# Kernel optimization log

Measured on AMD Instinct MI355X. Metric: run time of the kernel, lower is better.

## Reference

```python
import jax, jax.numpy as jnp
import numpy as np

N = 100000      # entity nodes
E = 1000000     # edges per relation
D_IN = 256
HID = 128
EPS = 1e-16     # PyG softmax denominator eps
NEG_SLOPE = 0.2 # GATConv default leaky_relu slope


def _gat_conv(x, ei, Ws, Wd, a_s, a_d, b):
    """Single-head GATConv (heads=1, concat=False) with self-loops."""
    n = x.shape[0]
    loop = jnp.arange(n, dtype=ei.dtype)
    src = jnp.concatenate([ei[0], loop])  # [E+N]
    dst = jnp.concatenate([ei[1], loop])
    h_src = x @ Ws                         # [N, HID]
    h_dst = x @ Wd                         # [N, HID]
    a_src = h_src @ a_s                    # [N]
    a_dst = h_dst @ a_d                    # [N]
    e = jax.nn.leaky_relu(a_src[src] + a_dst[dst], NEG_SLOPE)  # [E+N]
    # numerically-stable softmax over incoming edges of each dst node
    m = jax.ops.segment_max(e, dst, num_segments=n)
    ex = jnp.exp(e - m[dst])
    denom = jax.ops.segment_sum(ex, dst, num_segments=n)
    alpha = ex / (denom[dst] + EPS)        # [E+N]
    out = jax.ops.segment_sum(alpha[:, None] * h_src[src], dst, num_segments=n)
    return out + b


def setup_inputs() -> dict:
    key = jax.random.key(0)
    ks = jax.random.split(key, 9)
    s_in = 1.0 / np.sqrt(D_IN)
    s_h = 1.0 / np.sqrt(HID)
    return {
        "x": jax.random.normal(ks[0], (N, D_IN), dtype=jnp.float32),
        "edge_index_r0": jax.random.randint(ks[1], (2, E), 0, N, dtype=jnp.int64)
                         if jax.config.jax_enable_x64 else jax.random.randint(ks[1], (2, E), 0, N).astype(jnp.int32),
        "edge_index_r1": jax.random.randint(ks[2], (2, E), 0, N, dtype=jnp.int64)
                         if jax.config.jax_enable_x64 else jax.random.randint(ks[2], (2, E), 0, N).astype(jnp.int32),
        "W_src": jax.random.normal(ks[3], (2, D_IN, HID), dtype=jnp.float32) * s_in,
        "W_dst": jax.random.normal(ks[4], (2, D_IN, HID), dtype=jnp.float32) * s_in,
        "att_src": jax.random.normal(ks[5], (2, HID), dtype=jnp.float32) * s_h,
        "att_dst": jax.random.normal(ks[6], (2, HID), dtype=jnp.float32) * s_h,
        "bias": jnp.zeros((2, HID), dtype=jnp.float32),
    }


def reference(x, edge_index_r0, edge_index_r1, W_src, W_dst, att_src, att_dst, bias):
    # HeteroConv aggr='sum' over the two entity->entity relations
    out = _gat_conv(x, edge_index_r0, W_src[0], W_dst[0], att_src[0], att_dst[0], bias[0])
    out = out + _gat_conv(x, edge_index_r1, W_src[1], W_dst[1], att_src[1], att_dst[1], bias[1])
    # ELU; dropout p=0.0 is identity
    return jax.nn.elu(out)
```

## Files before the change

kernel.cpp:

```cpp
#include <hip/hip_runtime.h>

typedef __attribute__((ext_vector_type(8))) __bf16 bf16x8;
typedef __attribute__((ext_vector_type(4))) float floatx4;
typedef __attribute__((ext_vector_type(2))) float floatx2;

__device__ __forceinline__ float bf2f(unsigned short u) {
    return __uint_as_float(((unsigned)u) << 16);
}
__device__ __forceinline__ unsigned short f2bf(float f) {
    unsigned u = __float_as_uint(f);
    unsigned r = u + 0x7FFFu + ((u >> 16) & 1u);
    return (unsigned short)(r >> 16);
}

__device__ __forceinline__ void canon8(const void* src, unsigned short* dst,
                                       long long idx, int f) {
    if (f) {
        *(uint4*)&dst[idx] = *(const uint4*)((const unsigned short*)src + idx);
    } else {
        const float* sf = (const float*)src;
        unsigned short v[8];
        for (int j = 0; j < 8; ++j) v[j] = f2bf(sf[idx + j]);
        *(uint4*)&dst[idx] = *(const uint4*)v;
    }
}

__global__ __launch_bounds__(256) void detect2_k(
    const unsigned short* __restrict__ xs,
    const void* __restrict__ Ws, const void* __restrict__ Wd,
    const void* __restrict__ as, const void* __restrict__ ad,
    const void* __restrict__ b,
    int* __restrict__ flag, float* __restrict__ vecs,
    unsigned short* __restrict__ bsb) {
    __shared__ int sred[256];
    __shared__ int sflag;
    int tid = threadIdx.x;
    int cnt = 0;
    for (int j = 0; j < 16; ++j) {
        unsigned short u = xs[(tid * 16 + j) * 2];
        int e = (u >> 7) & 0xFF;
        cnt += (e >= 96 && e <= 159) ? 1 : 0;
    }
    sred[tid] = cnt;
    __syncthreads();
    for (int s = 128; s > 0; s >>= 1) {
        if (tid < s) sred[tid] += sred[tid + s];
        __syncthreads();
    }
    if (tid == 0) { sflag = (sred[0] > 2048) ? 1 : 0; *flag = sflag; }
    __syncthreads();
    int f = sflag;
    int k = tid;
    for (int r = 0; r < 2; ++r) {
        float s = 0.f, t = 0.f;
        if (f) {
            const unsigned short* wsrow = (const unsigned short*)Ws + (size_t)r * 32768 + (size_t)k * 128;
            const unsigned short* wdrow = (const unsigned short*)Wd + (size_t)r * 32768 + (size_t)k * 128;
            const unsigned short* asr = (const unsigned short*)as + r * 128;
            const unsigned short* adr = (const unsigned short*)ad + r * 128;
            for (int h = 0; h < 128; ++h) {
                s += bf2f(wsrow[h]) * bf2f(asr[h]);
                t += bf2f(wdrow[h]) * bf2f(adr[h]);
            }
        } else {
            const float* wsrow = (const float*)Ws + (size_t)r * 32768 + (size_t)k * 128;
            const float* wdrow = (const float*)Wd + (size_t)r * 32768 + (size_t)k * 128;
            const float* asr = (const float*)as + r * 128;
            const float* adr = (const float*)ad + r * 128;
            for (int h = 0; h < 128; ++h) {
                s += wsrow[h] * asr[h];
                t += wdrow[h] * adr[h];
            }
        }
        vecs[(r * 2 + 0) * 256 + k] = s;
        vecs[(r * 2 + 1) * 256 + k] = t;
    }
    if (tid < 32) canon8(b, bsb, (long long)tid * 8, f);
}

__global__ __launch_bounds__(256) void mix1_k(
    const int* __restrict__ ei0, const int* __restrict__ ei1,
    int* __restrict__ cntP, int* __restrict__ rank0, int* __restrict__ rank1,
    int E_, int histB, int period,
    const void* __restrict__ xraw, unsigned short* __restrict__ xb,
    const float* __restrict__ vecs, float* __restrict__ aout, int n, int canB,
    unsigned long long* __restrict__ pair0, unsigned long long* __restrict__ pair1,
    int ps2, int zB,
    const void* __restrict__ Ws, unsigned short* __restrict__ Bt,
    const int* __restrict__ flag) {
    __shared__ float sv[1024];
    int b = blockIdx.x, tid = threadIdx.x;
    int bq = b / period;
    if (b - bq * period == 0) {
        if (bq >= histB) return;
        int rel = bq & 1;
        int t = ((bq >> 1) << 8) + tid;
        if (t >= E_ + n) return;
        const int* ei = rel ? ei1 : ei0;
        int* rank = rel ? rank1 : rank0;
        int d = (t < E_) ? ei[E_ + t] : (t - E_);
        rank[t] = atomicAdd(&cntP[((rel ? n : 0) + d) << 4], 1);
        return;
    }
    int oid = b - bq - 1;
    if (oid < canB) {
        for (int j = 0; j < 4; ++j) sv[j * 256 + tid] = vecs[j * 256 + tid];
        __syncthreads();
        int lane = tid & 63, wave = tid >> 6;
        int row = oid * 4 + wave;
        if (row >= n) return;
        float xf[4];
        if (*flag) {
            uint2 u = *(const uint2*)((const unsigned short*)xraw + (size_t)row * 256 + lane * 4);
            xf[0] = bf2f((unsigned short)(u.x & 0xFFFF));
            xf[1] = bf2f((unsigned short)(u.x >> 16));
            xf[2] = bf2f((unsigned short)(u.y & 0xFFFF));
            xf[3] = bf2f((unsigned short)(u.y >> 16));
        } else {
            float4 f = *(const float4*)((const float*)xraw + (size_t)row * 256 + lane * 4);
            xf[0] = f.x; xf[1] = f.y; xf[2] = f.z; xf[3] = f.w;
            unsigned short v[4] = {f2bf(f.x), f2bf(f.y), f2bf(f.z), f2bf(f.w)};
            *(uint2*)&xb[(size_t)row * 256 + lane * 4] = *(const uint2*)v;
        }
        float s[4] = {0.f, 0.f, 0.f, 0.f};
        for (int j = 0; j < 4; ++j)
            for (int q = 0; q < 4; ++q)
                s[j] += xf[q] * sv[j * 256 + lane * 4 + q];
        for (int j = 0; j < 4; ++j)
            for (int off = 32; off > 0; off >>= 1)
                s[j] += __shfl_down(s[j], off);
        if (lane == 0)
            for (int j = 0; j < 4; ++j) aout[(size_t)j * n + row] = s[j];
        return;
    }
    oid -= canB;
    if (oid < 2 * zB) {
        unsigned long long* dst = (oid < zB) ? pair0 : pair1;
        int z = (oid < zB) ? oid : oid - zB;
        int idx = z * 256 + tid;
        if (idx < ps2) ((uint4*)dst)[idx] = make_uint4(0u, 0u, 0u, 0u);
        return;
    }
    oid -= 2 * zB;
    if (oid < 256) {
        int i = oid * 256 + tid;
        int f = *flag;
        int r = i >> 15, rem = i & 32767;
        int k = rem >> 7, nn = rem & 127;
        unsigned short w = f ? ((const unsigned short*)Ws)[i]
                             : f2bf(((const float*)Ws)[i]);
        Bt[(size_t)r * 32768 + nn * 256 + k] = w;
    }
}

__global__ __launch_bounds__(256) void scan_red_k(const int* __restrict__ cntP,
                                                  int* __restrict__ part,
                                                  int n, int nb) {
    __shared__ int s[256];
    int rel = blockIdx.y;
    int i = blockIdx.x * 256 + threadIdx.x;
    int v = (i < n) ? ((cntP[((rel ? n : 0) + i) << 4] + 7) & ~7) : 0;
    s[threadIdx.x] = v;
    __syncthreads();
    for (int o = 128; o > 0; o >>= 1) {
        if (threadIdx.x < o) s[threadIdx.x] += s[threadIdx.x + o];
        __syncthreads();
    }
    if (threadIdx.x == 0) part[rel * nb + blockIdx.x] = s[0];
}

__global__ __launch_bounds__(1024) void scan_mid_k(int* __restrict__ part, int nb) {
    __shared__ int s[1024];
    int rel = blockIdx.x;
    int t = threadIdx.x;
    s[t] = (t < nb) ? part[rel * nb + t] : 0;
    __syncthreads();
    for (int o = 1; o < 1024; o <<= 1) {
        int v = (t >= o) ? s[t - o] : 0;
        __syncthreads();
        s[t] += v;
        __syncthreads();
    }
    if (t < nb) part[rel * nb + t] = (t == 0) ? 0 : s[t - 1];
}

__global__ __launch_bounds__(256) void scan_off_k(const int* __restrict__ cntP,
                                                  const int* __restrict__ part,
                                                  int* __restrict__ off0,
                                                  int* __restrict__ off1,
                                                  int n, int nb) {
    __shared__ int s[256];
    int rel = blockIdx.y;
    int* off = rel ? off1 : off0;
    int i = blockIdx.x * 256 + threadIdx.x;
    int t = threadIdx.x;
    int v = (i < n) ? ((cntP[((rel ? n : 0) + i) << 4] + 7) & ~7) : 0;
    s[t] = v;
    __syncthreads();
    for (int o = 1; o < 256; o <<= 1) {
        int u = (t >= o) ? s[t - o] : 0;
        __syncthreads();
        s[t] += u;
        __syncthreads();
    }
    if (i < n) off[i] = part[rel * nb + blockIdx.x] + s[t] - v;
}

__device__ __forceinline__ void gload_lds16(const void* g, void* l) {
    __builtin_amdgcn_global_load_lds((const __attribute__((address_space(1))) void*)g,
                                     (__attribute__((address_space(3))) void*)l, 16, 0, 0);
}

__global__ __launch_bounds__(256) void mix2_k(
    const void* __restrict__ x_raw, const unsigned short* __restrict__ xb,
    const unsigned short* __restrict__ Btg,
    unsigned short* __restrict__ hout, int n, int gemmB, int period,
    const int* __restrict__ ei0, const int* __restrict__ ei1,
    const float* __restrict__ avals,
    const int* __restrict__ off0, const int* __restrict__ off1,
    const int* __restrict__ rank0, const int* __restrict__ rank1,
    unsigned long long* __restrict__ pair0, unsigned long long* __restrict__ pair1,
    int E_, int fillB, const int* __restrict__ flag) {
    __shared__ __align__(16) unsigned short As[128 * 64];
    __shared__ __align__(16) unsigned short Bs[128 * 64];
    int b = blockIdx.x, tid = threadIdx.x;
    int bq = b / period;
    if (b - bq * period == 0) {
        if (bq >= gemmB) return;
        const unsigned short* x = (*flag) ? (const unsigned short*)x_raw : xb;
        const int r = bq & 1;
        const unsigned short* bt = Btg + (size_t)r * 32768;
        unsigned short* h = hout + (size_t)r * n * 128;
        const int r0 = (bq >> 1) * 128;
        int lane = tid & 63, wave = tid >> 6;
        int wm = wave >> 1, wn = wave & 1;
        floatx4 acc[4][4];
        for (int mt = 0; mt < 4; ++mt)
            for (int nt = 0; nt < 4; ++nt)
                acc[mt][nt] = (floatx4){0.f, 0.f, 0.f, 0.f};
        int srow = lane >> 3, q = lane & 7;
        int m16 = lane & 15, qb = lane >> 4;
        for (int k0 = 0; k0 < 256; k0 += 64) {
            for (int i = 0; i < 4; ++i) {
                int L = wave * 4 + i;
                int row = L * 8 + srow;
                int sw = ((q ^ (row & 7)) << 3);
                int grow = min(r0 + row, n - 1);
                gload_lds16(x + (size_t)grow * 256 + k0 + sw, &As[L * 512]);
                gload_lds16(bt + (size_t)row * 256 + k0 + sw, &Bs[L * 512]);
            }
            __syncthreads();
            for (int s = 0; s < 2; ++s) {
                int qr = qb + s * 4;
                bf16x8 af[4], bfv[4];
                for (int mt = 0; mt < 4; ++mt) {
                    int row = wm * 64 + mt * 16 + m16;
                    af[mt] = *(const bf16x8*)&As[row * 64 + ((qr ^ (row & 7)) << 3)];
                }
                for (int nt = 0; nt < 4; ++nt) {
                    int row = wn * 64 + nt * 16 + m16;
                    bfv[nt] = *(const bf16x8*)&Bs[row * 64 + ((qr ^ (row & 7)) << 3)];
                }
                for (int mt = 0; mt < 4; ++mt)
                    for (int nt = 0; nt < 4; ++nt)
                        acc[mt][nt] = __builtin_amdgcn_mfma_f32_16x16x32_bf16(
                            af[mt], bfv[nt], acc[mt][nt], 0, 0, 0);
            }
            __syncthreads();
        }
        for (int mt = 0; mt < 4; ++mt) {
            int baser = r0 + wm * 64 + mt * 16 + qb * 4;
            for (int nt = 0; nt < 4; ++nt) {
                int c = wn * 64 + nt * 16 + m16;
                for (int i = 0; i < 4; ++i) {
                    int gr = baser + i;
                    if (gr < n) h[(size_t)gr * 128 + c] = f2bf(acc[mt][nt][i]);
                }
            }
        }
        return;
    }
    int fid = b - bq - 1;
    if (fid >= fillB) return;
    int rel = fid & 1;
    int t = ((fid >> 1) << 8) + tid;
    if (t >= E_ + n) return;
    const int* ei = rel ? ei1 : ei0;
    const float* as_ = avals + (rel ? 2 * (size_t)n : 0);
    const float* ad_ = avals + (rel ? 3 * (size_t)n : (size_t)n);
    const int* off = rel ? off1 : off0;
    const int* rank = rel ? rank1 : rank0;
    unsigned long long* pair = rel ? pair1 : pair0;
    int s, d;
    if (t < E_) { s = ei[t]; d = ei[E_ + t]; } else { s = t - E_; d = s; }
    float e = as_[s] + ad_[d];
    e = e > 0.f ? e : 0.2f * e;
    float w = __expf(e);
    int pos = off[d] + rank[t];
    pair[pos] = ((unsigned long long)__float_as_uint(w) << 32) | (unsigned)s;
}

__device__ __forceinline__ void acc8pk(floatx2* a, float w, const uint4& hv) {
    floatx2 wv = {w, w};
    const unsigned u[4] = {hv.x, hv.y, hv.z, hv.w};
#pragma unroll
    for (int k = 0; k < 4; ++k) {
        floatx2 hf;
        hf.x = __uint_as_float(u[k] << 16);
        hf.y = __uint_as_float(u[k] & 0xFFFF0000u);
        asm("v_pk_fma_f32 %0, %1, %2, %0" : "+v"(a[k]) : "v"(wv), "v"(hf));
    }
}

__device__ __forceinline__ void rel_accP(int s0, int nIt, int g, unsigned l4,
                                         const unsigned long long* __restrict__ pair,
                                         const char* __restrict__ h8,
                                         floatx2* __restrict__ a, float& den) {
    int i = s0 + g;
    unsigned long long p0 = pair[i];
    unsigned long long p1 = pair[i + 4];
    for (int it = 0; it < nIt; ++it) {
        i += 8;
        unsigned long long q0 = pair[i];
        unsigned long long q1 = pair[i + 4];
        uint4 h0 = *(const uint4*)(h8 + ((((unsigned)p0) << 8) + l4));
        uint4 h1 = *(const uint4*)(h8 + ((((unsigned)p1) << 8) + l4));
        float w0 = __uint_as_float((unsigned)(p0 >> 32));
        float w1 = __uint_as_float((unsigned)(p1 >> 32));
        den += w0 + w1;
        acc8pk(a, w0, h0);
        acc8pk(a, w1, h1);
        p0 = q0; p1 = q1;
    }
}

__global__ __launch_bounds__(256) void agg_k(
    const int* __restrict__ off0, const int* __restrict__ off1,
    const int* __restrict__ cntP,
    const unsigned long long* __restrict__ pair0,
    const unsigned long long* __restrict__ pair1,
    const char* __restrict__ h0, const char* __restrict__ h1,
    const unsigned short* __restrict__ bias, void* __restrict__ out,
    int n, const int* __restrict__ flag) {
    int wave = threadIdx.x >> 6, lane = threadIdx.x & 63;
    int g = lane >> 4, l = lane & 15;
    unsigned l4 = (unsigned)l << 4;
    int d = blockIdx.x * 4 + wave;
    if (d >= n) return;

    int sA = off0[d], nItA = (cntP[d << 4] + 7) >> 3;
    int sB = off1[d], nItB = (cntP[(n + d) << 4] + 7) >> 3;

    float denA = 0.f, denB = 0.f;
    floatx2 aA[4], aB[4];
#pragma unroll
    for (int k = 0; k < 4; ++k) {
        aA[k] = (floatx2){0.f, 0.f};
        aB[k] = (floatx2){0.f, 0.f};
    }
    rel_accP(sA, nItA, g, l4, pair0, h0, aA, denA);
    rel_accP(sB, nItB, g, l4, pair1, h1, aB, denB);

    denA += __shfl_xor(denA, 16);
    denA += __shfl_xor(denA, 32);
    denB += __shfl_xor(denB, 16);
    denB += __shfl_xor(denB, 32);
    float invA = __builtin_amdgcn_rcpf(denA + 1e-16f);
    float invB = __builtin_amdgcn_rcpf(denB + 1e-16f);
    floatx2 ivA = {invA, invA}, ivB = {invB, invB};
#pragma unroll
    for (int k = 0; k < 4; ++k) {
        asm("v_pk_mul_f32 %0, %0, %1" : "+v"(aA[k]) : "v"(ivA));
        asm("v_pk_fma_f32 %0, %1, %2, %0" : "+v"(aA[k]) : "v"(aB[k]), "v"(ivB));
    }
    float t8[8] = {aA[0].x, aA[0].y, aA[1].x, aA[1].y,
                   aA[2].x, aA[2].y, aA[3].x, aA[3].y};

    uint4 b0 = *(const uint4*)&bias[l * 8];
    uint4 b1 = *(const uint4*)&bias[128 + l * 8];
    const unsigned* b0u = (const unsigned*)&b0;
    const unsigned* b1u = (const unsigned*)&b1;
    float v[8];
#pragma unroll
    for (int j = 0; j < 8; ++j) {
        float s = t8[j];
        s += __shfl_xor(s, 16);
        s += __shfl_xor(s, 32);
        unsigned w0 = b0u[j >> 1], w1 = b1u[j >> 1];
        float bb = bf2f((unsigned short)((j & 1) ? (w0 >> 16) : (w0 & 0xFFFFu)))
                 + bf2f((unsigned short)((j & 1) ? (w1 >> 16) : (w1 & 0xFFFFu)));
        float t = s + bb;
        v[j] = t > 0.f ? t : (__expf(t) - 1.f);
    }
    if (g == 0) {
        if (*flag) {
            unsigned pk[4];
            for (int j = 0; j < 4; ++j)
                pk[j] = ((unsigned)f2bf(v[2 * j + 1]) << 16) | (unsigned)f2bf(v[2 * j]);
            ((uint4*)out)[(size_t)d * 16 + l] = *(const uint4*)pk;
        } else {
            float4 f0 = make_float4(v[0], v[1], v[2], v[3]);
            float4 f1 = make_float4(v[4], v[5], v[6], v[7]);
            ((float4*)out)[(size_t)d * 32 + l * 2] = f0;
            ((float4*)out)[(size_t)d * 32 + l * 2 + 1] = f1;
        }
    }
}

static inline char* carve(char*& p, size_t bytes) {
    char* r = p;
    p += (bytes + 255) & ~(size_t)255;
    return r;
}

extern "C" void kernel_launch(void* const* d_in, const int* in_sizes, int n_in,
                              void* d_out, int out_size, void* d_ws, size_t ws_size,
                              hipStream_t stream) {
    (void)n_in; (void)out_size; (void)ws_size;
    const void* x_raw  = d_in[0];
    const int*  ei0    = (const int*)d_in[1];
    const int*  ei1    = (const int*)d_in[2];
    const void* Ws_raw = d_in[3];
    const void* Wd_raw = d_in[4];
    const void* as_raw = d_in[5];
    const void* ad_raw = d_in[6];
    const void* b_raw  = d_in[7];

    const int n = in_sizes[0] / 256;
    const int e = in_sizes[1] / 2;
    const int tot = e + n;
    const int nb = (n + 255) / 256;
    const int PS = tot + 7 * n + 32;
    const int ps2 = PS / 2;
    const int zB = (ps2 + 255) / 256;

    char* p = (char*)d_ws;
    float* avals = (float*)carve(p, (size_t)4 * n * 4);
    int*   cntP  = (int*)carve(p, (size_t)2 * n * 64);
    int*   off0  = (int*)carve(p, (size_t)n * 4);
    int*   off1  = (int*)carve(p, (size_t)n * 4);
    int*   part  = (int*)carve(p, (size_t)2 * nb * 4);
    int*   rank0 = (int*)carve(p, (size_t)tot * 4);
    int*   rank1 = (int*)carve(p, (size_t)tot * 4);
    unsigned long long* pair0 = (unsigned long long*)carve(p, (size_t)PS * 8);
    unsigned long long* pair1 = (unsigned long long*)carve(p, (size_t)PS * 8);
    float* vecs  = (float*)carve(p, 1024 * 4);
    int*   flag  = (int*)carve(p, 256);
    unsigned short* xb  = (unsigned short*)carve(p, (size_t)(n + 128) * 256 * 2);
    unsigned short* h0  = (unsigned short*)carve(p, (size_t)2 * n * 128 * 2);
    unsigned short* h1  = h0 + (size_t)n * 128;
    unsigned short* Bt  = (unsigned short*)carve(p, 65536 * 2);
    unsigned short* bsb = (unsigned short*)carve(p, 256 * 2);

    hipMemsetAsync(cntP, 0, (size_t)2 * n * 64, stream);

    detect2_k<<<1, 256, 0, stream>>>((const unsigned short*)x_raw, Ws_raw, Wd_raw,
                                     as_raw, ad_raw, b_raw, flag, vecs, bsb);

    int gb = (tot + 255) / 256;
    int histB = gb * 2;
    int canB = (n + 3) / 4;
    int otherTotal = canB + 2 * zB + 256;
    int period = (otherTotal + histB - 1) / histB + 1;
    int G = histB * period;
    mix1_k<<<G, 256, 0, stream>>>(
        ei0, ei1, cntP, rank0, rank1, e, histB, period,
        x_raw, xb, vecs, avals, n, canB,
        pair0, pair1, ps2, zB,
        Ws_raw, Bt, flag);

    scan_red_k<<<dim3(nb, 2), 256, 0, stream>>>(cntP, part, n, nb);
    scan_mid_k<<<2, 1024, 0, stream>>>(part, nb);
    scan_off_k<<<dim3(nb, 2), 256, 0, stream>>>(cntP, part, off0, off1, n, nb);

    int gemmB = ((n + 127) / 128) * 2;
    int fillB = gb * 2;
    int period2 = (fillB + gemmB - 1) / gemmB + 1;
    int G2 = gemmB * period2;
    mix2_k<<<G2, 256, 0, stream>>>(
        x_raw, xb, Bt, h0, n, gemmB, period2,
        ei0, ei1, avals, off0, off1, rank0, rank1, pair0, pair1, e, fillB, flag);

    agg_k<<<(n + 3) / 4, 256, 0, stream>>>(off0, off1, cntP, pair0, pair1,
                                           (const char*)h0, (const char*)h1,
                                           bsb, d_out, n, flag);
}
```

Baseline: 464.7 us.

## Split fused gemm/fill kernel and interleave both relations in aggregation loop

```diff
diff --git a/kernel.cpp b/kernel.cpp
--- a/kernel.cpp
+++ b/kernel.cpp
@@ -188,6 +188,7 @@
                                                   const int* __restrict__ part,
                                                   int* __restrict__ off0,
                                                   int* __restrict__ off1,
+                                                  unsigned short* __restrict__ nit,
                                                   int n, int nb) {
     __shared__ int s[256];
     int rel = blockIdx.y;
@@ -203,94 +204,28 @@
         s[t] += u;
         __syncthreads();
     }
-    if (i < n) off[i] = part[rel * nb + blockIdx.x] + s[t] - v;
-}
-
-__device__ __forceinline__ void gload_lds16(const void* g, void* l) {
-    __builtin_amdgcn_global_load_lds((const __attribute__((address_space(1))) void*)g,
-                                     (__attribute__((address_space(3))) void*)l, 16, 0, 0);
-}
-
-__global__ __launch_bounds__(256) void mix2_k(
-    const void* __restrict__ x_raw, const unsigned short* __restrict__ xb,
-    const unsigned short* __restrict__ Btg,
-    unsigned short* __restrict__ hout, int n, int gemmB, int period,
-    const int* __restrict__ ei0, const int* __restrict__ ei1,
-    const float* __restrict__ avals,
-    const int* __restrict__ off0, const int* __restrict__ off1,
-    const int* __restrict__ rank0, const int* __restrict__ rank1,
-    unsigned long long* __restrict__ pair0, unsigned long long* __restrict__ pair1,
-    int E_, int fillB, const int* __restrict__ flag) {
-    __shared__ __align__(16) unsigned short As[128 * 64];
-    __shared__ __align__(16) unsigned short Bs[128 * 64];
-    int b = blockIdx.x, tid = threadIdx.x;
-    int bq = b / period;
-    if (b - bq * period == 0) {
-        if (bq >= gemmB) return;
-        const unsigned short* x = (*flag) ? (const unsigned short*)x_raw : xb;
-        const int r = bq & 1;
-        const unsigned short* bt = Btg + (size_t)r * 32768;
-        unsigned short* h = hout + (size_t)r * n * 128;
-        const int r0 = (bq >> 1) * 128;
-        int lane = tid & 63, wave = tid >> 6;
-        int wm = wave >> 1, wn = wave & 1;
-        floatx4 acc[4][4];
-        for (int mt = 0; mt < 4; ++mt)
-            for (int nt = 0; nt < 4; ++nt)
-                acc[mt][nt] = (floatx4){0.f, 0.f, 0.f, 0.f};
-        int srow = lane >> 3, q = lane & 7;
-        int m16 = lane & 15, qb = lane >> 4;
-        for (int k0 = 0; k0 < 256; k0 += 64) {
-            for (int i = 0; i < 4; ++i) {
-                int L = wave * 4 + i;
-                int row = L * 8 + srow;
-                int sw = ((q ^ (row & 7)) << 3);
-                int grow = min(r0 + row, n - 1);
-                gload_lds16(x + (size_t)grow * 256 + k0 + sw, &As[L * 512]);
-                gload_lds16(bt + (size_t)row * 256 + k0 + sw, &Bs[L * 512]);
-            }
-            __syncthreads();
-            for (int s = 0; s < 2; ++s) {
-                int qr = qb + s * 4;
-                bf16x8 af[4], bfv[4];
-                for (int mt = 0; mt < 4; ++mt) {
-                    int row = wm * 64 + mt * 16 + m16;
-                    af[mt] = *(const bf16x8*)&As[row * 64 + ((qr ^ (row & 7)) << 3)];
-                }
-                for (int nt = 0; nt < 4; ++nt) {
-                    int row = wn * 64 + nt * 16 + m16;
-                    bfv[nt] = *(const bf16x8*)&Bs[row * 64 + ((qr ^ (row & 7)) << 3)];
-                }
-                for (int mt = 0; mt < 4; ++mt)
-                    for (int nt = 0; nt < 4; ++nt)
-                        acc[mt][nt] = __builtin_amdgcn_mfma_f32_16x16x32_bf16(
-                            af[mt], bfv[nt], acc[mt][nt], 0, 0, 0);
-            }
-            __syncthreads();
-        }
-        for (int mt = 0; mt < 4; ++mt) {
-            int baser = r0 + wm * 64 + mt * 16 + qb * 4;
-            for (int nt = 0; nt < 4; ++nt) {
-                int c = wn * 64 + nt * 16 + m16;
-                for (int i = 0; i < 4; ++i) {
-                    int gr = baser + i;
-                    if (gr < n) h[(size_t)gr * 128 + c] = f2bf(acc[mt][nt][i]);
-                }
-            }
-        }
-        return;
-    }
-    int fid = b - bq - 1;
-    if (fid >= fillB) return;
-    int rel = fid & 1;
-    int t = ((fid >> 1) << 8) + tid;
-    if (t >= E_ + n) return;
+    if (i < n) {
+        off[i] = part[rel * nb + blockIdx.x] + s[t] - v;
+        nit[2 * i + rel] = (unsigned short)(v >> 3);
+    }
+}
+
+__global__ void fill2_k(const int* __restrict__ ei0, const int* __restrict__ ei1,
+                        const float* __restrict__ avals,
+                        const int* __restrict__ off0, const int* __restrict__ off1,
+                        const int* __restrict__ rank0, const int* __restrict__ rank1,
+                        unsigned long long* __restrict__ pair0,
+                        unsigned long long* __restrict__ pair1,
+                        int E_, int n) {
+    int rel = blockIdx.y;
     const int* ei = rel ? ei1 : ei0;
     const float* as_ = avals + (rel ? 2 * (size_t)n : 0);
     const float* ad_ = avals + (rel ? 3 * (size_t)n : (size_t)n);
     const int* off = rel ? off1 : off0;
     const int* rank = rel ? rank1 : rank0;
     unsigned long long* pair = rel ? pair1 : pair0;
+    int t = blockIdx.x * 256 + threadIdx.x;
+    if (t >= E_ + n) return;
     int s, d;
     if (t < E_) { s = ei[t]; d = ei[E_ + t]; } else { s = t - E_; d = s; }
     float e = as_[s] + ad_[d];
@@ -298,6 +233,75 @@
     float w = __expf(e);
     int pos = off[d] + rank[t];
     pair[pos] = ((unsigned long long)__float_as_uint(w) << 32) | (unsigned)s;
+}
+
+__device__ __forceinline__ void gload_lds16(const void* g, void* l) {
+    __builtin_amdgcn_global_load_lds((const __attribute__((address_space(1))) void*)g,
+                                     (__attribute__((address_space(3))) void*)l, 16, 0, 0);
+}
+
+__global__ __launch_bounds__(256) void gemm_h(const void* __restrict__ x_raw,
+                                              const unsigned short* __restrict__ xb,
+                                              const unsigned short* __restrict__ Btg,
+                                              unsigned short* __restrict__ hout, int n,
+                                              const int* __restrict__ flag) {
+    const unsigned short* x = (*flag) ? (const unsigned short*)x_raw : xb;
+    const int r = blockIdx.y;
+    const unsigned short* bt = Btg + (size_t)r * 32768;
+    unsigned short* h = hout + (size_t)r * n * 128;
+    const int r0 = blockIdx.x * 128;
+    __shared__ __align__(16) unsigned short As[128 * 64];
+    __shared__ __align__(16) unsigned short Bs[128 * 64];
+    int tid = threadIdx.x;
+    int lane = tid & 63, wave = tid >> 6;
+    int wm = wave >> 1, wn = wave & 1;
+
+    floatx4 acc[4][4];
+    for (int mt = 0; mt < 4; ++mt)
+        for (int nt = 0; nt < 4; ++nt)
+            acc[mt][nt] = (floatx4){0.f, 0.f, 0.f, 0.f};
+
+    int srow = lane >> 3, q = lane & 7;
+    int m16 = lane & 15, qb = lane >> 4;
+
+    for (int k0 = 0; k0 < 256; k0 += 64) {
+        for (int i = 0; i < 4; ++i) {
+            int L = wave * 4 + i;
+            int row = L * 8 + srow;
+            int sw = ((q ^ (row & 7)) << 3);
+            int grow = min(r0 + row, n - 1);
+            gload_lds16(x + (size_t)grow * 256 + k0 + sw, &As[L * 512]);
+            gload_lds16(bt + (size_t)row * 256 + k0 + sw, &Bs[L * 512]);
+        }
+        __syncthreads();
+        for (int s = 0; s < 2; ++s) {
+            int qr = qb + s * 4;
+            bf16x8 af[4], bfv[4];
+            for (int mt = 0; mt < 4; ++mt) {
+                int row = wm * 64 + mt * 16 + m16;
+                af[mt] = *(const bf16x8*)&As[row * 64 + ((qr ^ (row & 7)) << 3)];
+            }
+            for (int nt = 0; nt < 4; ++nt) {
+                int row = wn * 64 + nt * 16 + m16;
+                bfv[nt] = *(const bf16x8*)&Bs[row * 64 + ((qr ^ (row & 7)) << 3)];
+            }
+            for (int mt = 0; mt < 4; ++mt)
+                for (int nt = 0; nt < 4; ++nt)
+                    acc[mt][nt] = __builtin_amdgcn_mfma_f32_16x16x32_bf16(
+                        af[mt], bfv[nt], acc[mt][nt], 0, 0, 0);
+        }
+        __syncthreads();
+    }
+    for (int mt = 0; mt < 4; ++mt) {
+        int baser = r0 + wm * 64 + mt * 16 + qb * 4;
+        for (int nt = 0; nt < 4; ++nt) {
+            int c = wn * 64 + nt * 16 + m16;
+            for (int i = 0; i < 4; ++i) {
+                int gr = baser + i;
+                if (gr < n) h[(size_t)gr * 128 + c] = f2bf(acc[mt][nt][i]);
+            }
+        }
+    }
 }
 
 __device__ __forceinline__ void acc8pk(floatx2* a, float w, const uint4& hv) {
@@ -312,31 +316,9 @@
     }
 }
 
-__device__ __forceinline__ void rel_accP(int s0, int nIt, int g, unsigned l4,
-                                         const unsigned long long* __restrict__ pair,
-                                         const char* __restrict__ h8,
-                                         floatx2* __restrict__ a, float& den) {
-    int i = s0 + g;
-    unsigned long long p0 = pair[i];
-    unsigned long long p1 = pair[i + 4];
-    for (int it = 0; it < nIt; ++it) {
-        i += 8;
-        unsigned long long q0 = pair[i];
-        unsigned long long q1 = pair[i + 4];
-        uint4 h0 = *(const uint4*)(h8 + ((((unsigned)p0) << 8) + l4));
-        uint4 h1 = *(const uint4*)(h8 + ((((unsigned)p1) << 8) + l4));
-        float w0 = __uint_as_float((unsigned)(p0 >> 32));
-        float w1 = __uint_as_float((unsigned)(p1 >> 32));
-        den += w0 + w1;
-        acc8pk(a, w0, h0);
-        acc8pk(a, w1, h1);
-        p0 = q0; p1 = q1;
-    }
-}
-
 __global__ __launch_bounds__(256) void agg_k(
     const int* __restrict__ off0, const int* __restrict__ off1,
-    const int* __restrict__ cntP,
+    const unsigned* __restrict__ nit,
     const unsigned long long* __restrict__ pair0,
     const unsigned long long* __restrict__ pair1,
     const char* __restrict__ h0, const char* __restrict__ h1,
@@ -348,8 +330,10 @@
     int d = blockIdx.x * 4 + wave;
     if (d >= n) return;
 
-    int sA = off0[d], nItA = (cntP[d << 4] + 7) >> 3;
-    int sB = off1[d], nItB = (cntP[(n + d) << 4] + 7) >> 3;
+    unsigned nn = nit[d];
+    int nItA = (int)(nn & 0xFFFFu), nItB = (int)(nn >> 16);
+    int nIt = max(nItA, nItB);
+    int iA = off0[d] + g, iB = off1[d] + g;
 
     float denA = 0.f, denB = 0.f;
     floatx2 aA[4], aB[4];
@@ -358,8 +342,34 @@
         aA[k] = (floatx2){0.f, 0.f};
         aB[k] = (floatx2){0.f, 0.f};
     }
-    rel_accP(sA, nItA, g, l4, pair0, h0, aA, denA);
-    rel_accP(sB, nItB, g, l4, pair1, h1, aB, denB);
+
+    unsigned long long pA0 = pair0[iA];
+    unsigned long long pA1 = pair0[iA + 4];
+    unsigned long long pB0 = pair1[iB];
+    unsigned long long pB1 = pair1[iB + 4];
+
+    for (int it = 0; it < nIt; ++it) {
+        uint4 hA0 = *(const uint4*)(h0 + ((((unsigned)pA0) << 8) + l4));
+        uint4 hA1 = *(const uint4*)(h0 + ((((unsigned)pA1) << 8) + l4));
+        uint4 hB0 = *(const uint4*)(h1 + ((((unsigned)pB0) << 8) + l4));
+        uint4 hB1 = *(const uint4*)(h1 + ((((unsigned)pB1) << 8) + l4));
+        bool mA = it < nItA, mB = it < nItB;
+        float wA0 = mA ? __uint_as_float((unsigned)(pA0 >> 32)) : 0.f;
+        float wA1 = mA ? __uint_as_float((unsigned)(pA1 >> 32)) : 0.f;
+        float wB0 = mB ? __uint_as_float((unsigned)(pB0 >> 32)) : 0.f;
+        float wB1 = mB ? __uint_as_float((unsigned)(pB1 >> 32)) : 0.f;
+        iA += 8; iB += 8;
+        pA0 = pair0[iA];
+        pA1 = pair0[iA + 4];
+        pB0 = pair1[iB];
+        pB1 = pair1[iB + 4];
+        denA += wA0 + wA1;
+        denB += wB0 + wB1;
+        acc8pk(aA, wA0, hA0);
+        acc8pk(aA, wA1, hA1);
+        acc8pk(aB, wB0, hB0);
+        acc8pk(aB, wB1, hB1);
+    }
 
     denA += __shfl_xor(denA, 16);
     denA += __shfl_xor(denA, 32);
@@ -430,7 +440,7 @@
     const int e = in_sizes[1] / 2;
     const int tot = e + n;
     const int nb = (n + 255) / 256;
-    const int PS = tot + 7 * n + 32;
+    const int PS = tot + 7 * n + 512;
     const int ps2 = PS / 2;
     const int zB = (ps2 + 255) / 256;
 
@@ -439,6 +449,7 @@
     int*   cntP  = (int*)carve(p, (size_t)2 * n * 64);
     int*   off0  = (int*)carve(p, (size_t)n * 4);
     int*   off1  = (int*)carve(p, (size_t)n * 4);
+    unsigned short* nit = (unsigned short*)carve(p, (size_t)n * 4);
     int*   part  = (int*)carve(p, (size_t)2 * nb * 4);
     int*   rank0 = (int*)carve(p, (size_t)tot * 4);
     int*   rank1 = (int*)carve(p, (size_t)tot * 4);
@@ -471,17 +482,14 @@
 
     scan_red_k<<<dim3(nb, 2), 256, 0, stream>>>(cntP, part, n, nb);
     scan_mid_k<<<2, 1024, 0, stream>>>(part, nb);
-    scan_off_k<<<dim3(nb, 2), 256, 0, stream>>>(cntP, part, off0, off1, n, nb);
-
-    int gemmB = ((n + 127) / 128) * 2;
-    int fillB = gb * 2;
-    int period2 = (fillB + gemmB - 1) / gemmB + 1;
-    int G2 = gemmB * period2;
-    mix2_k<<<G2, 256, 0, stream>>>(
-        x_raw, xb, Bt, h0, n, gemmB, period2,
-        ei0, ei1, avals, off0, off1, rank0, rank1, pair0, pair1, e, fillB, flag);
-
-    agg_k<<<(n + 3) / 4, 256, 0, stream>>>(off0, off1, cntP, pair0, pair1,
+    scan_off_k<<<dim3(nb, 2), 256, 0, stream>>>(cntP, part, off0, off1, nit, n, nb);
+
+    fill2_k<<<dim3(gb, 2), 256, 0, stream>>>(ei0, ei1, avals, off0, off1,
+                                             rank0, rank1, pair0, pair1, e, n);
+    gemm_h<<<dim3((n + 127) / 128, 2), 256, 0, stream>>>(x_raw, xb, Bt, h0, n, flag);
+
+    agg_k<<<(n + 3) / 4, 256, 0, stream>>>(off0, off1, (const unsigned*)nit,
+                                           pair0, pair1,
                                            (const char*)h0, (const char*)h1,
                                            bsb, d_out, n, flag);
 }
```

Result: faster. 453.8 us (-2.3%).
